# Kernel optimization log

Measured on AMD Instinct MI355X. Metric: run time of the kernel, lower is better.

Reference implementation:

```python
import jax, jax.numpy as jnp
import numpy as np
from jax import lax

B, IN_CH, OUT_CH, H, W_SP, K, PAD = 4, 64, 128, 56, 56, 3, 1


def setup_inputs() -> dict:
    key = jax.random.key(0)
    k1, k2, k3 = jax.random.split(key, 3)
    x = jax.random.normal(k1, (B, IN_CH, H, W_SP), dtype=jnp.float32)
    W = jax.random.normal(k2, (OUT_CH, IN_CH, K, K), dtype=jnp.float32) * 0.05
    b = jax.random.normal(k3, (OUT_CH,), dtype=jnp.float32) * 0.05
    return {"x": x, "W": W, "b": b}


def reference(x, W, b):
    in_ch, out_ch = W.shape[1], W.shape[0]
    # make_preadd_conv: grouped (depthwise-expanded) conv with groups=in_ch.
    # Permuted kernel order: preadd channel p = i*out_ch + j uses kernel W[j, i].
    rhs = jnp.transpose(W, (1, 0, 2, 3)).reshape(in_ch * out_ch, 1, K, K)  # OIHW
    preadd = lax.conv_general_dilated(
        x, rhs,
        window_strides=(1, 1),
        padding=((PAD, PAD), (PAD, PAD)),
        feature_group_count=in_ch,
        dimension_numbers=("NCHW", "OIHW", "NCHW"),
    )  # [B, in_ch*out_ch, H, W]
    bsz, _, h, w = preadd.shape
    # permute_add_featuremaps: out channel o = sum_i preadd[:, i*out_ch + o]
    added = preadd.reshape(bsz, in_ch, out_ch, h, w).sum(axis=1)
    return added + b[:, None, None]
```

## Files before the change

### kernel.cpp

```cpp
#include <hip/hip_runtime.h>
#include <hip/hip_bf16.h>

#define BATCH 4
#define IC 64
#define OC 128
#define HSZ 56
#define WSZ 56
#define HW 3136
#define KTOT 576
#define GUARD 64
#define XPIX (HW + 2*GUARD)

typedef __attribute__((ext_vector_type(8))) short bf16x8;
typedef __attribute__((ext_vector_type(4))) float f32x4;

__global__ __launch_bounds__(256) void prep_kernel(
    const float* __restrict__ x,
    const float* __restrict__ W,
    unsigned short* __restrict__ Wb,
    unsigned short* __restrict__ xbf)
{
    const int blk = blockIdx.x;
    const int t   = threadIdx.x;

    if (blk < BATCH * 51) {
        const int b    = blk / 51;
        const int tile = blk - b * 51;
        const int px   = (t & 63);
        const int chg  = t >> 6;
        const int gp   = tile * 64 - GUARD + px;
        const bool inb = (unsigned)gp < (unsigned)HW;
        const float* xb = x + (size_t)b * IC * HW;

        unsigned short __attribute__((aligned(16))) v[16];
#pragma unroll
        for (int i = 0; i < 16; ++i) {
            const int ch = chg * 16 + i;
            float f = inb ? xb[ch * HW + gp] : 0.0f;
            __hip_bfloat16 h = __float2bfloat16(f);
            v[i] = *reinterpret_cast<unsigned short*>(&h);
        }
        unsigned short* dst = xbf + ((size_t)b * XPIX + (gp + GUARD)) * IC + chg * 16;
        *reinterpret_cast<uint4*>(dst)     = *reinterpret_cast<uint4*>(&v[0]);
        *reinterpret_cast<uint4*>(dst + 8) = *reinterpret_cast<uint4*>(&v[8]);
    } else {
        const int j = (blk - BATCH * 51) * 256 + t;
        if (j < OC * KTOT) {
            const int o   = j / KTOT;
            const int k   = j - o * KTOT;
            const int tap = k >> 6;
            const int ch  = k & 63;
            __hip_bfloat16 h = __float2bfloat16(W[(o * IC + ch) * 9 + tap]);
            Wb[j] = *reinterpret_cast<unsigned short*>(&h);
        }
    }
}

__global__ __launch_bounds__(256) void conv_mfma_kernel(
    const unsigned short* __restrict__ xbf,
    const unsigned short* __restrict__ Wb,
    const float* __restrict__ bias,
    float* __restrict__ out)
{
    const int t    = threadIdx.x;
    const int lane = t & 63;
    const int pg   = t >> 6;
    const int lrow = lane & 15;
    const int lk   = lane >> 4;

    const int p0 = blockIdx.x * 64;
    const int og = blockIdx.y;
    const int b  = blockIdx.z;

    const int apix = p0 + pg * 16 + lrow;
    const int ah = apix / WSZ;
    const int aw = apix - ah * WSZ;

    unsigned vmask = 0;
#pragma unroll
    for (int tp = 0; tp < 9; ++tp) {
        const int hh = ah + (tp / 3) - 1;
        const int ww = aw + (tp % 3) - 1;
        if ((unsigned)hh < (unsigned)HSZ && (unsigned)ww < (unsigned)WSZ)
            vmask |= (1u << tp);
    }

    const unsigned short* xa = xbf + ((size_t)b * XPIX + GUARD + apix) * IC + lk * 8;
    const unsigned short* wb = Wb + (size_t)(og * 64 + lrow) * KTOT + lk * 8;

    f32x4 acc[4] = {{0,0,0,0},{0,0,0,0},{0,0,0,0},{0,0,0,0}};
    const bf16x8 zfrag = {0,0,0,0,0,0,0,0};

#pragma unroll
    for (int tp = 0; tp < 9; ++tp) {
        const int toff = ((tp / 3) - 1) * WSZ + ((tp % 3) - 1);
        const bool valid = (vmask >> tp) & 1u;
        const unsigned short* xrow = xa + toff * IC;
#pragma unroll
        for (int half = 0; half < 2; ++half) {
            bf16x8 a = *reinterpret_cast<const bf16x8*>(xrow + half * 32);
            a = valid ? a : zfrag;
            const unsigned short* wp = wb + tp * 64 + half * 32;
            bf16x8 b0 = *reinterpret_cast<const bf16x8*>(wp);
            bf16x8 b1 = *reinterpret_cast<const bf16x8*>(wp + 16 * KTOT);
            bf16x8 b2 = *reinterpret_cast<const bf16x8*>(wp + 32 * KTOT);
            bf16x8 b3 = *reinterpret_cast<const bf16x8*>(wp + 48 * KTOT);
            acc[0] = __builtin_amdgcn_mfma_f32_16x16x32_bf16(a, b0, acc[0], 0, 0, 0);
            acc[1] = __builtin_amdgcn_mfma_f32_16x16x32_bf16(a, b1, acc[1], 0, 0, 0);
            acc[2] = __builtin_amdgcn_mfma_f32_16x16x32_bf16(a, b2, acc[2], 0, 0, 0);
            acc[3] = __builtin_amdgcn_mfma_f32_16x16x32_bf16(a, b3, acc[3], 0, 0, 0);
        }
    }

    const int pstore = p0 + pg * 16 + 4 * lk;
#pragma unroll
    for (int bg = 0; bg < 4; ++bg) {
        const int o = og * 64 + bg * 16 + lrow;
        f32x4 r = acc[bg] + bias[o];
        *reinterpret_cast<f32x4*>(&out[((size_t)(b * OC + o)) * HW + pstore]) = r;
    }
}

extern "C" void kernel_launch(void* const* d_in, const int* in_sizes, int n_in,
                              void* d_out, int out_size, void* d_ws, size_t ws_size,
                              hipStream_t stream) {
    const float* x    = (const float*)d_in[0];
    const float* W    = (const float*)d_in[1];
    const float* bias = (const float*)d_in[2];
    float* out        = (float*)d_out;

    unsigned short* Wb  = (unsigned short*)d_ws;
    unsigned short* xbf = (unsigned short*)((char*)d_ws + 147456);

    const int wblocks = (OC * KTOT + 255) / 256;
    prep_kernel<<<BATCH * 51 + wblocks, 256, 0, stream>>>(x, W, Wb, xbf);

    dim3 grid(HW / 64, 2, BATCH);
    conv_mfma_kernel<<<grid, 256, 0, stream>>>(xbf, Wb, bias, out);
}
```

Baseline: 32.57 us.

## Use zero-padded input layout and 64x64 per-wave MFMA tiles

The input is stored as a zero-padded 58-wide image in bf16, which removes the per-tap validity masks in the conv kernel. Each wave now computes a 64-pixel by 64-channel tile (4x4 MFMA accumulators) instead of 16x64, so each weight fragment is reused across four pixel groups. The grid shrinks to 27x2x4 blocks of 128 threads, about 216 blocks. Outputs become scalar stores with padding checks instead of vector stores, and the border pixels do wasted work.

After: 34.51 us. 1.06x slower.

```diff
diff --git a/kernel.cpp b/kernel.cpp
--- a/kernel.cpp
+++ b/kernel.cpp
@@ -7,9 +7,11 @@
 #define HSZ 56
 #define WSZ 56
 #define HW 3136
+#define PW 58
+#define PPIX 3364
 #define KTOT 576
-#define GUARD 64
-#define XPIX (HW + 2*GUARD)
+#define GROWS 64
+#define XROWS 3584
 
 typedef __attribute__((ext_vector_type(8))) short bf16x8;
 typedef __attribute__((ext_vector_type(4))) float f32x4;
@@ -18,33 +20,40 @@
     const float* __restrict__ x,
     const float* __restrict__ W,
     unsigned short* __restrict__ Wb,
-    unsigned short* __restrict__ xbf)
+    unsigned short* __restrict__ xpad)
 {
     const int blk = blockIdx.x;
     const int t   = threadIdx.x;
 
-    if (blk < BATCH * 51) {
-        const int b    = blk / 51;
-        const int tile = blk - b * 51;
-        const int px   = (t & 63);
+    if (blk < BATCH * 56) {
+        const int b    = blk / 56;
+        const int tile = blk - b * 56;
+        const int a    = tile * 64 + (t & 63);
         const int chg  = t >> 6;
-        const int gp   = tile * 64 - GUARD + px;
-        const bool inb = (unsigned)gp < (unsigned)HW;
+        const int pp   = a - GROWS;
+        int r = 1, c = 1;
+        bool inb = false;
+        if (pp >= 0 && pp < PPIX) {
+            r = pp / PW;
+            c = pp - r * PW;
+            inb = (r >= 1) && (r <= HSZ) && (c >= 1) && (c <= WSZ);
+        }
+        const int sp = (r - 1) * WSZ + (c - 1);
         const float* xb = x + (size_t)b * IC * HW;
 
         unsigned short __attribute__((aligned(16))) v[16];
 #pragma unroll
         for (int i = 0; i < 16; ++i) {
             const int ch = chg * 16 + i;
-            float f = inb ? xb[ch * HW + gp] : 0.0f;
+            float f = inb ? xb[ch * HW + sp] : 0.0f;
             __hip_bfloat16 h = __float2bfloat16(f);
             v[i] = *reinterpret_cast<unsigned short*>(&h);
         }
-        unsigned short* dst = xbf + ((size_t)b * XPIX + (gp + GUARD)) * IC + chg * 16;
+        unsigned short* dst = xpad + ((size_t)b * XROWS + a) * IC + chg * 16;
         *reinterpret_cast<uint4*>(dst)     = *reinterpret_cast<uint4*>(&v[0]);
         *reinterpret_cast<uint4*>(dst + 8) = *reinterpret_cast<uint4*>(&v[8]);
     } else {
-        const int j = (blk - BATCH * 51) * 256 + t;
+        const int j = (blk - BATCH * 56) * 256 + t;
         if (j < OC * KTOT) {
             const int o   = j / KTOT;
             const int k   = j - o * KTOT;
@@ -56,68 +65,86 @@
     }
 }
 
-__global__ __launch_bounds__(256) void conv_mfma_kernel(
-    const unsigned short* __restrict__ xbf,
+__global__ __launch_bounds__(128) void conv_mfma_kernel(
+    const unsigned short* __restrict__ xpad,
     const unsigned short* __restrict__ Wb,
     const float* __restrict__ bias,
     float* __restrict__ out)
 {
     const int t    = threadIdx.x;
     const int lane = t & 63;
-    const int pg   = t >> 6;
+    const int wv   = t >> 6;
     const int lrow = lane & 15;
     const int lk   = lane >> 4;
 
-    const int p0 = blockIdx.x * 64;
-    const int og = blockIdx.y;
-    const int b  = blockIdx.z;
+    const int pw0 = blockIdx.x * 128 + wv * 64;
+    const int og  = blockIdx.y;
+    const int b   = blockIdx.z;
 
-    const int apix = p0 + pg * 16 + lrow;
-    const int ah = apix / WSZ;
-    const int aw = apix - ah * WSZ;
+    const unsigned short* xb = xpad + ((size_t)b * XROWS + GROWS) * IC;
+    const unsigned short* xa0 = xb + (size_t)(pw0 +  0 + lrow) * IC + lk * 8;
+    const unsigned short* xa1 = xb + (size_t)(pw0 + 16 + lrow) * IC + lk * 8;
+    const unsigned short* xa2 = xb + (size_t)(pw0 + 32 + lrow) * IC + lk * 8;
+    const unsigned short* xa3 = xb + (size_t)(pw0 + 48 + lrow) * IC + lk * 8;
+    const unsigned short* wbp = Wb + (size_t)(og * 64 + lrow) * KTOT + lk * 8;
 
-    unsigned vmask = 0;
-#pragma unroll
-    for (int tp = 0; tp < 9; ++tp) {
-        const int hh = ah + (tp / 3) - 1;
-        const int ww = aw + (tp % 3) - 1;
-        if ((unsigned)hh < (unsigned)HSZ && (unsigned)ww < (unsigned)WSZ)
-            vmask |= (1u << tp);
-    }
-
-    const unsigned short* xa = xbf + ((size_t)b * XPIX + GUARD + apix) * IC + lk * 8;
-    const unsigned short* wb = Wb + (size_t)(og * 64 + lrow) * KTOT + lk * 8;
-
-    f32x4 acc[4] = {{0,0,0,0},{0,0,0,0},{0,0,0,0},{0,0,0,0}};
-    const bf16x8 zfrag = {0,0,0,0,0,0,0,0};
+    f32x4 acc[4][4] = {};
 
 #pragma unroll
-    for (int tp = 0; tp < 9; ++tp) {
-        const int toff = ((tp / 3) - 1) * WSZ + ((tp % 3) - 1);
-        const bool valid = (vmask >> tp) & 1u;
-        const unsigned short* xrow = xa + toff * IC;
+    for (int dh = -1; dh <= 1; ++dh) {
 #pragma unroll
-        for (int half = 0; half < 2; ++half) {
-            bf16x8 a = *reinterpret_cast<const bf16x8*>(xrow + half * 32);
-            a = valid ? a : zfrag;
-            const unsigned short* wp = wb + tp * 64 + half * 32;
-            bf16x8 b0 = *reinterpret_cast<const bf16x8*>(wp);
-            bf16x8 b1 = *reinterpret_cast<const bf16x8*>(wp + 16 * KTOT);
-            bf16x8 b2 = *reinterpret_cast<const bf16x8*>(wp + 32 * KTOT);
-            bf16x8 b3 = *reinterpret_cast<const bf16x8*>(wp + 48 * KTOT);
-            acc[0] = __builtin_amdgcn_mfma_f32_16x16x32_bf16(a, b0, acc[0], 0, 0, 0);
-            acc[1] = __builtin_amdgcn_mfma_f32_16x16x32_bf16(a, b1, acc[1], 0, 0, 0);
-            acc[2] = __builtin_amdgcn_mfma_f32_16x16x32_bf16(a, b2, acc[2], 0, 0, 0);
-            acc[3] = __builtin_amdgcn_mfma_f32_16x16x32_bf16(a, b3, acc[3], 0, 0, 0);
+        for (int dw = -1; dw <= 1; ++dw) {
+            const int toff = dh * PW + dw;
+            const int tap  = (dh + 1) * 3 + (dw + 1);
+#pragma unroll
+            for (int half = 0; half < 2; ++half) {
+                const int ao = toff * IC + half * 32;
+                bf16x8 a0 = *reinterpret_cast<const bf16x8*>(xa0 + ao);
+                bf16x8 a1 = *reinterpret_cast<const bf16x8*>(xa1 + ao);
+                bf16x8 a2 = *reinterpret_cast<const bf16x8*>(xa2 + ao);
+                bf16x8 a3 = *reinterpret_cast<const bf16x8*>(xa3 + ao);
+                const unsigned short* wp = wbp + tap * 64 + half * 32;
+                bf16x8 b0 = *reinterpret_cast<const bf16x8*>(wp);
+                bf16x8 b1 = *reinterpret_cast<const bf16x8*>(wp + 16 * KTOT);
+                bf16x8 b2 = *reinterpret_cast<const bf16x8*>(wp + 32 * KTOT);
+                bf16x8 b3 = *reinterpret_cast<const bf16x8*>(wp + 48 * KTOT);
+                acc[0][0] = __builtin_amdgcn_mfma_f32_16x16x32_bf16(a0, b0, acc[0][0], 0, 0, 0);
+                acc[0][1] = __builtin_amdgcn_mfma_f32_16x16x32_bf16(a0, b1, acc[0][1], 0, 0, 0);
+                acc[0][2] = __builtin_amdgcn_mfma_f32_16x16x32_bf16(a0, b2, acc[0][2], 0, 0, 0);
+                acc[0][3] = __builtin_amdgcn_mfma_f32_16x16x32_bf16(a0, b3, acc[0][3], 0, 0, 0);
+                acc[1][0] = __builtin_amdgcn_mfma_f32_16x16x32_bf16(a1, b0, acc[1][0], 0, 0, 0);
+                acc[1][1] = __builtin_amdgcn_mfma_f32_16x16x32_bf16(a1, b1, acc[1][1], 0, 0, 0);
+                acc[1][2] = __builtin_amdgcn_mfma_f32_16x16x32_bf16(a1, b2, acc[1][2], 0, 0, 0);
+                acc[1][3] = __builtin_amdgcn_mfma_f32_16x16x32_bf16(a1, b3, acc[1][3], 0, 0, 0);
+                acc[2][0] = __builtin_amdgcn_mfma_f32_16x16x32_bf16(a2, b0, acc[2][0], 0, 0, 0);
+                acc[2][1] = __builtin_amdgcn_mfma_f32_16x16x32_bf16(a2, b1, acc[2][1], 0, 0, 0);
+                acc[2][2] = __builtin_amdgcn_mfma_f32_16x16x32_bf16(a2, b2, acc[2][2], 0, 0, 0);
+                acc[2][3] = __builtin_amdgcn_mfma_f32_16x16x32_bf16(a2, b3, acc[2][3], 0, 0, 0);
+                acc[3][0] = __builtin_amdgcn_mfma_f32_16x16x32_bf16(a3, b0, acc[3][0], 0, 0, 0);
+                acc[3][1] = __builtin_amdgcn_mfma_f32_16x16x32_bf16(a3, b1, acc[3][1], 0, 0, 0);
+                acc[3][2] = __builtin_amdgcn_mfma_f32_16x16x32_bf16(a3, b2, acc[3][2], 0, 0, 0);
+                acc[3][3] = __builtin_amdgcn_mfma_f32_16x16x32_bf16(a3, b3, acc[3][3], 0, 0, 0);
+            }
         }
     }
 
-    const int pstore = p0 + pg * 16 + 4 * lk;
 #pragma unroll
     for (int bg = 0; bg < 4; ++bg) {
-        const int o = og * 64 + bg * 16 + lrow;
-        f32x4 r = acc[bg] + bias[o];
-        *reinterpret_cast<f32x4*>(&out[((size_t)(b * OC + o)) * HW + pstore]) = r;
+        const int oc = og * 64 + bg * 16 + lrow;
+        const float bv = bias[oc];
+        float* ob = out + ((size_t)(b * OC + oc)) * HW;
+#pragma unroll
+        for (int mg = 0; mg < 4; ++mg) {
+            const int pbase = pw0 + mg * 16 + 4 * lk;
+#pragma unroll
+            for (int j = 0; j < 4; ++j) {
+                const int p = pbase + j;
+                const int r = p / PW;
+                const int c = p - r * PW;
+                if (r >= 1 && r <= HSZ && c >= 1 && c <= WSZ)
+                    ob[(r - 1) * WSZ + (c - 1)] = acc[mg][bg][j] + bv;
+            }
+        }
     }
 }
 
@@ -129,12 +156,11 @@
     const float* bias = (const float*)d_in[2];
     float* out        = (float*)d_out;
 
-    unsigned short* Wb  = (unsigned short*)d_ws;
-    unsigned short* xbf = (unsigned short*)((char*)d_ws + 147456);
+    unsigned short* Wb   = (unsigned short*)d_ws;
+    unsigned short* xpad = (unsigned short*)((char*)d_ws + 147456);
 
-    const int wblocks = (OC * KTOT + 255) / 256;
-    prep_kernel<<<BATCH * 51 + wblocks, 256, 0, stream>>>(x, W, Wb, xbf);
+    prep_kernel<<<BATCH * 56 + (OC * KTOT + 255) / 256, 256, 0, stream>>>(x, W, Wb, xpad);
 
-    dim3 grid(HW / 64, 2, BATCH);
-    conv_mfma_kernel<<<grid, 256, 0, stream>>>(xbf, Wb, bias, out);
+    dim3 grid(27, 2, BATCH);
+    conv_mfma_kernel<<<grid, 128, 0, stream>>>(xpad, Wb, bias, out);
 }
```
